# Kernel optimization log

Measured on AMD Instinct MI355X. Metric: run time of the kernel, lower is better.

Reference implementation:

```python
import jax, jax.numpy as jnp
import numpy as np
from jax import lax

D_MODEL = 256
N_LAYERS = 4
D_STATE = 64
EXPAND = 2
HEADDIM = 64
D_CONV = 4
D_INNER = EXPAND * D_MODEL                      # 512
NHEADS = D_INNER // HEADDIM                     # 8
CONV_DIM = D_INNER + 2 * D_STATE                # 640 (ngroups=1)
D_IN_PROJ = 2 * D_INNER + 2 * D_STATE + NHEADS  # 1160
B_SZ, SEQ = 8, 2048


def _silu(x):
    return x * jax.nn.sigmoid(x)


def _mamba2(u, W_in, W_conv, b_conv, dt_bias, A_log, Dp, norm_w, W_out):
    # Standard Mamba2 block (in_proj -> causal depthwise conv -> selective scan
    # with per-head scalar A -> gated RMSNorm -> out_proj).
    B, L, _ = u.shape
    zxbcdt = u @ W_in.T                                   # [B,L,1160]
    z = zxbcdt[..., :D_INNER]
    xBC = zxbcdt[..., D_INNER:D_INNER + CONV_DIM]
    dt = jax.nn.softplus(zxbcdt[..., D_INNER + CONV_DIM:] + dt_bias)  # [B,L,H]
    # causal depthwise conv1d + silu
    xc = lax.conv_general_dilated(xBC.transpose(0, 2, 1), W_conv[:, None, :],
                                  (1,), [(D_CONV - 1, 0)],
                                  dimension_numbers=('NCH', 'OIH', 'NCH'),
                                  feature_group_count=CONV_DIM)
    xBC = _silu(xc.transpose(0, 2, 1) + b_conv)
    x = xBC[..., :D_INNER].reshape(B, L, NHEADS, HEADDIM)
    Bm = xBC[..., D_INNER:D_INNER + D_STATE]              # [B,L,N]
    Cm = xBC[..., D_INNER + D_STATE:]                     # [B,L,N]
    dA = jnp.exp(dt * (-jnp.exp(A_log)))                  # [B,L,H]

    def step(h, inp):
        dA_t, dt_t, x_t, B_t, C_t = inp
        # h: [B,H,P,N]
        h = dA_t[:, :, None, None] * h + (dt_t[:, :, None] * x_t)[..., None] * B_t[:, None, None, :]
        y = jnp.einsum('bhpn,bn->bhp', h, C_t)
        return h, y

    h0 = jnp.zeros((B, NHEADS, HEADDIM, D_STATE), u.dtype)
    xs = (dA.transpose(1, 0, 2), dt.transpose(1, 0, 2), x.transpose(1, 0, 2, 3),
          Bm.transpose(1, 0, 2), Cm.transpose(1, 0, 2))
    _, ys = lax.scan(step, h0, xs)                        # [L,B,H,P]
    y = ys.transpose(1, 0, 2, 3) + Dp[None, None, :, None] * x
    y = y.reshape(B, L, D_INNER)
    y = y * _silu(z)                                      # gate before RMSNorm
    y = y * lax.rsqrt(jnp.mean(y * y, axis=-1, keepdims=True) + 1e-5) * norm_w
    return y @ W_out.T


def _encoder(x, pf, pb):
    for i in range(N_LAYERS - 1):
        y_fwd = _mamba2(x, *[p[i] for p in pf])
        y_bwd = _mamba2(x[:, ::-1], *[p[i] for p in pb])[:, ::-1]
        x = y_fwd + y_bwd
    h_fwd = _mamba2(x, *[p[-1] for p in pf])
    h_bwd = _mamba2(x[:, ::-1], *[p[-1] for p in pb])[:, ::-1]
    H = (h_fwd + h_bwd).mean(axis=1)
    return h_fwd, h_bwd, H


def _make_params(key):
    k = jax.random.split(key, 4)
    W_in = jax.random.normal(k[0], (N_LAYERS, D_IN_PROJ, D_MODEL), jnp.float32) * 0.02
    W_conv = jax.random.normal(k[1], (N_LAYERS, CONV_DIM, D_CONV), jnp.float32) * 0.2
    b_conv = jnp.zeros((N_LAYERS, CONV_DIM), jnp.float32)
    dt = jnp.exp(jax.random.uniform(k[2], (N_LAYERS, NHEADS)) * (np.log(0.1) - np.log(0.001)) + np.log(0.001))
    dt_bias = dt + jnp.log(-jnp.expm1(-dt))               # softplus^{-1}(dt)
    A_log = jnp.log(jax.random.uniform(k[3], (N_LAYERS, NHEADS), minval=1.0, maxval=16.0))
    Dp = jnp.ones((N_LAYERS, NHEADS), jnp.float32)
    norm_w = jnp.ones((N_LAYERS, D_INNER), jnp.float32)
    W_out = jax.random.normal(jax.random.fold_in(k[0], 7), (N_LAYERS, D_MODEL, D_INNER), jnp.float32) * 0.02
    return (W_in, W_conv, b_conv, dt_bias, A_log, Dp, norm_w, W_out)


def setup_inputs():
    key = jax.random.key(0)
    kx, kf, kb = jax.random.split(key, 3)
    x = jax.random.normal(kx, (B_SZ, SEQ, D_MODEL), jnp.float32)
    pf = _make_params(kf)
    pb = _make_params(kb)
    names = ['Win', 'Wconv', 'bconv', 'dt_bias', 'A_log', 'D', 'norm_w', 'Wout']
    inp = {'x_conditioned': x}
    for n, p in zip(names, pf):
        inp[n + '_f'] = p
    for n, p in zip(names, pb):
        inp[n + '_b'] = p
    return inp


def reference(x_conditioned, Win_f, Wconv_f, bconv_f, dt_bias_f, A_log_f, D_f, norm_w_f, Wout_f,
              Win_b, Wconv_b, bconv_b, dt_bias_b, A_log_b, D_b, norm_w_b, Wout_b):
    pf = (Win_f, Wconv_f, bconv_f, dt_bias_f, A_log_f, D_f, norm_w_f, Wout_f)
    pb = (Win_b, Wconv_b, bconv_b, dt_bias_b, A_log_b, D_b, norm_w_b, Wout_b)
    return _encoder(x_conditioned, pf, pb)
```

## Files before the change

### kernel.cpp

```cpp
#include <hip/hip_runtime.h>
#include <math.h>


#define TC 64
#define NC 32
#define SPITCH 72
#define HIOFF 8388608

#define ZB_STR   8388608u
#define XBCB_STR 10485760u
#define HINP_STR 16777216u
#define XCP_STR  10485760u
#define DT_STR   131072u
#define SB_STR   131072u
#define PT_STR   2048u

typedef __attribute__((ext_vector_type(4))) float f32x4;
typedef __attribute__((ext_vector_type(8))) short s16x8;

#define MFMA __builtin_amdgcn_mfma_f32_16x16x32_bf16

__device__ __forceinline__ float siluf(float x) { return x / (1.f + expf(-x)); }

__device__ __forceinline__ ushort f2b(float f) {
  union { float f; uint u; } v; v.f = f;
  return (ushort)((v.u + 0x7FFFu + ((v.u >> 16) & 1u)) >> 16);
}
__device__ __forceinline__ float b2f(ushort u) {
  union { uint u; float f; } v; v.u = ((uint)u) << 16; return v.f;
}
__device__ __forceinline__ int swz(int r, int c) { return c ^ (r & 3) ^ ((r >> 2) & 3); }

__device__ __forceinline__ int soff(int base, int r, int cc) {
  return base + r * SPITCH + ((((cc >> 3) ^ (r & 7) ^ ((r >> 3) & 7)) << 3) | (cc & 7));
}
__device__ __forceinline__ int toff(int base, int r, int cc) {
  return base + r * 64 + ((((cc >> 3) ^ (r & 7)) << 3) | (cc & 7));
}

__device__ __forceinline__ uint packf(float y) {
  const ushort hb = f2b(y);
  const ushort lb = f2b(y - b2f(hb));
  return (uint)hb | ((uint)lb << 16);
}
__device__ __forceinline__ float unpackf(uint u) {
  return b2f((ushort)(u & 0xffffu)) + b2f((ushort)(u >> 16));
}

__device__ __forceinline__ void unzip8(const uint4 u0, const uint4 u1, s16x8& hh, s16x8& ll) {
  const uint a[8] = {u0.x, u0.y, u0.z, u0.w, u1.x, u1.y, u1.z, u1.w};
#pragma unroll
  for (int e = 0; e < 8; ++e) {
    hh[e] = (short)(a[e] & 0xffffu);
    ll[e] = (short)(a[e] >> 16);
  }
}

__device__ __forceinline__ void stage16p(ushort* tiles, const uint* src,
                                         int bh_, int bl_, int r, int c0) {
  const uint4 u0 = *(const uint4*)(src + c0);
  const uint4 u1 = *(const uint4*)(src + c0 + 4);
  const uint4 u2 = *(const uint4*)(src + c0 + 8);
  const uint4 u3 = *(const uint4*)(src + c0 + 12);
  s16x8 h0, l0, h1, l1;
  unzip8(u0, u1, h0, l0);
  unzip8(u2, u3, h1, l1);
  *(s16x8*)&tiles[toff(bh_, r, c0)]     = h0;
  *(s16x8*)&tiles[toff(bl_, r, c0)]     = l0;
  *(s16x8*)&tiles[toff(bh_, r, c0 + 8)] = h1;
  *(s16x8*)&tiles[toff(bl_, r, c0 + 8)] = l1;
}

__global__ __launch_bounds__(256) void k_cvt(
    const float* __restrict__ src, ushort* __restrict__ dst, int n8)
{
  const int i = blockIdx.x * 256 + threadIdx.x;
  if (i >= n8) return;
  const float4 v0 = *(const float4*)(src + (size_t)i * 8);
  const float4 v1 = *(const float4*)(src + (size_t)i * 8 + 4);
  s16x8 h;
#pragma unroll
  for (int e = 0; e < 4; ++e) h[e] = (short)f2b(((const float*)&v0)[e]);
#pragma unroll
  for (int e = 0; e < 4; ++e) h[e + 4] = (short)f2b(((const float*)&v1)[e]);
  *(s16x8*)(dst + (size_t)i * 8) = h;
}

__global__ __launch_bounds__(256) void k_gemmb(
    const ushort* __restrict__ A, const ushort* __restrict__ Winb, int layer,
    ushort* __restrict__ zb, ushort* __restrict__ xbc,
    const float* __restrict__ db0, const float* __restrict__ db1,
    const float* __restrict__ Al0, const float* __restrict__ Al1,
    float* __restrict__ dtb, float* __restrict__ dab)
{
  const int zd = blockIdx.z;
  const ushort* W = Winb + ((size_t)zd * 4 + layer) * 296960;
  zb  += (size_t)zd * ZB_STR;
  xbc += (size_t)zd * XBCB_STR;
  dtb += (size_t)zd * DT_STR;
  dab += (size_t)zd * DT_STR;
  const float* dt_bias = zd ? db1 : db0;
  const float* A_log   = zd ? Al1 : Al0;
  const int N = 1160, K = 256;

  __shared__ __align__(16) ushort lds[17408];
  const int tid = threadIdx.x;
  const int lane = tid & 63;
  const int wid = tid >> 6;
  const int wr = wid >> 1, wc = wid & 1;
  const int m0 = blockIdx.x * 128, n0 = blockIdx.y * 128;

  const int tr = tid >> 1;
  const int th = tid & 1;
  const int gm = m0 + tr;
  const int bb = gm >> 11, tt = gm & 2047;
  const int tphys = zd ? (2047 - tt) : tt;
  const ushort* Arow = A + (size_t)((bb << 11) + tphys) * 256 + th * 16;
  const int wn = n0 + tr;
  const ushort* Wrow = (wn < N) ? (W + (size_t)wn * K + th * 16) : nullptr;

  const int asw0 = tr * 32 + swz(tr, th * 2) * 8;
  const int asw1 = tr * 32 + swz(tr, th * 2 + 1) * 8;

  f32x4 acc[4][4];
#pragma unroll
  for (int i = 0; i < 4; ++i)
#pragma unroll
    for (int j = 0; j < 4; ++j) acc[i][j] = (f32x4){0.f, 0.f, 0.f, 0.f};

  int aoff[4], boff[4];
#pragma unroll
  for (int f = 0; f < 4; ++f) {
    const int ar = wr * 64 + f * 16 + (lane & 15);
    aoff[f] = ar * 32 + swz(ar, lane >> 4) * 8;
    const int br = wc * 64 + f * 16 + (lane & 15);
    boff[f] = 4096 + br * 32 + swz(br, lane >> 4) * 8;
  }

  const s16x8 zz = (s16x8){0, 0, 0, 0, 0, 0, 0, 0};
  s16x8 a0 = *(const s16x8*)(Arow);
  s16x8 a1 = *(const s16x8*)(Arow + 8);
  s16x8 b0 = zz, b1 = zz;
  if (Wrow) {
    b0 = *(const s16x8*)(Wrow);
    b1 = *(const s16x8*)(Wrow + 8);
  }

  for (int k0 = 0; k0 < K; k0 += 32) {
    __syncthreads();
    *(s16x8*)&lds[asw0] = a0;
    *(s16x8*)&lds[asw1] = a1;
    *(s16x8*)&lds[4096 + asw0] = b0;
    *(s16x8*)&lds[4096 + asw1] = b1;
    __syncthreads();
    if (k0 + 32 < K) {
      a0 = *(const s16x8*)(Arow + k0 + 32);
      a1 = *(const s16x8*)(Arow + k0 + 40);
      if (Wrow) {
        b0 = *(const s16x8*)(Wrow + k0 + 32);
        b1 = *(const s16x8*)(Wrow + k0 + 40);
      }
    }
    s16x8 af[4], bf[4];
#pragma unroll
    for (int f = 0; f < 4; ++f) {
      af[f] = *(const s16x8*)&lds[aoff[f]];
      bf[f] = *(const s16x8*)&lds[boff[f]];
    }
#pragma unroll
    for (int i = 0; i < 4; ++i)
#pragma unroll
      for (int j = 0; j < 4; ++j)
        acc[i][j] = MFMA(af[i], bf[j], acc[i][j], 0, 0, 0);
  }

  const int by = blockIdx.y;
  if (by == 9) {
    if (wc == 0 && (lane & 15) < 8) {
      const int cl = lane & 15;
      const float bias = dt_bias[cl];
      const float eAl = expf(A_log[cl]);
#pragma unroll
      for (int i = 0; i < 4; ++i) {
        const int r = m0 + wr * 64 + i * 16 + (lane >> 4) * 4;
#pragma unroll
        for (int g = 0; g < 4; ++g) {
          const float v = acc[i][0][g] + bias;
          const float sp = (v > 20.f) ? v : log1pf(expf(v));
          dtb[(size_t)(r + g) * 8 + cl] = sp;
          dab[(size_t)(r + g) * 8 + cl] = sp * eAl;
        }
      }
    }
    return;
  }
  __syncthreads();
#pragma unroll
  for (int i = 0; i < 4; ++i) {
    const int r = wr * 64 + i * 16 + (lane >> 4) * 4;
#pragma unroll
    for (int j = 0; j < 4; ++j) {
      const int ccol = wc * 64 + j * 16 + (lane & 15);
#pragma unroll
      for (int g = 0; g < 4; ++g)
        lds[(r + g) * 136 + ccol] = f2b(acc[i][j][g]);
    }
  }
  __syncthreads();
  const int rr = tid >> 1, hf = tid & 1;
  const int grow = m0 + rr;
  ushort* dst; int stride, colb;
  if (by < 4) { dst = zb;  stride = 512; colb = n0; }
  else        { dst = xbc; stride = 640; colb = n0 - 512; }
  ushort* dp = dst + (size_t)grow * stride + colb + hf * 64;
  const ushort* sp = &lds[rr * 136 + hf * 64];
#pragma unroll
  for (int q = 0; q < 8; ++q)
    *(s16x8*)(dp + q * 8) = *(const s16x8*)(sp + q * 8);
}

__global__ __launch_bounds__(256) void k_gemmo_mid(
    const ushort* __restrict__ ybf, const ushort* __restrict__ Woutb, int layer,
    ushort* __restrict__ xbf)
{
  __shared__ __align__(16) ushort lds[8192];
  const int tid = threadIdx.x;
  const int lane = tid & 63;
  const int wid = tid >> 6;
  const int wr = wid >> 1, wc = wid & 1;
  const int m0 = blockIdx.x * 128, n0 = blockIdx.y * 128;

  const int tr = tid >> 1;
  const int th = tid & 1;
  const int gm = m0 + tr;
  const int bb = gm >> 11, tt = gm & 2047;
  const int wn = n0 + tr;

  const int asw0 = tr * 32 + swz(tr, th * 2) * 8;
  const int asw1 = tr * 32 + swz(tr, th * 2 + 1) * 8;

  f32x4 acc[4][4];
#pragma unroll
  for (int i = 0; i < 4; ++i)
#pragma unroll
    for (int j = 0; j < 4; ++j) acc[i][j] = (f32x4){0.f, 0.f, 0.f, 0.f};

  int aoff[4], boff[4];
#pragma unroll
  for (int f = 0; f < 4; ++f) {
    const int ar = wr * 64 + f * 16 + (lane & 15);
    aoff[f] = ar * 32 + swz(ar, lane >> 4) * 8;
    const int br = wc * 64 + f * 16 + (lane & 15);
    boff[f] = 4096 + br * 32 + swz(br, lane >> 4) * 8;
  }

  for (int dir = 0; dir < 2; ++dir) {
    const int tphys = dir ? (2047 - tt) : tt;
    const ushort* Arow = ybf + (size_t)dir * ZB_STR
                       + (size_t)((bb << 11) + tphys) * 512 + th * 16;
    const ushort* Wrow = Woutb + ((size_t)dir * 4 + layer) * 131072
                       + (size_t)wn * 512 + th * 16;
    s16x8 a0 = *(const s16x8*)(Arow);
    s16x8 a1 = *(const s16x8*)(Arow + 8);
    s16x8 b0 = *(const s16x8*)(Wrow);
    s16x8 b1 = *(const s16x8*)(Wrow + 8);
    for (int k0 = 0; k0 < 512; k0 += 32) {
      __syncthreads();
      *(s16x8*)&lds[asw0] = a0;
      *(s16x8*)&lds[asw1] = a1;
      *(s16x8*)&lds[4096 + asw0] = b0;
      *(s16x8*)&lds[4096 + asw1] = b1;
      __syncthreads();
      if (k0 + 32 < 512) {
        a0 = *(const s16x8*)(Arow + k0 + 32);
        a1 = *(const s16x8*)(Arow + k0 + 40);
        b0 = *(const s16x8*)(Wrow + k0 + 32);
        b1 = *(const s16x8*)(Wrow + k0 + 40);
      }
      s16x8 af[4], bf[4];
#pragma unroll
      for (int f = 0; f < 4; ++f) {
        af[f] = *(const s16x8*)&lds[aoff[f]];
        bf[f] = *(const s16x8*)&lds[boff[f]];
      }
#pragma unroll
      for (int i = 0; i < 4; ++i)
#pragma unroll
        for (int j = 0; j < 4; ++j)
          acc[i][j] = MFMA(af[i], bf[j], acc[i][j], 0, 0, 0);
    }
  }

#pragma unroll
  for (int i = 0; i < 4; ++i) {
    const int rb = m0 + wr * 64 + i * 16 + (lane >> 4) * 4;
#pragma unroll
    for (int g = 0; g < 4; ++g) {
      const size_t rbase = (size_t)(rb + g) * 256 + n0 + wc * 64 + (lane & 15);
#pragma unroll
      for (int j = 0; j < 4; ++j)
        xbf[rbase + j * 16] = f2b(acc[i][j][g]);
    }
  }
}

__global__ __launch_bounds__(256) void k_gemmo_last(
    const ushort* __restrict__ ybf, const ushort* __restrict__ Woutb,
    float* __restrict__ hF, float* __restrict__ hB)
{
  const int zd = blockIdx.z;
  const ushort* A = ybf + (size_t)zd * ZB_STR;
  const ushort* W = Woutb + ((size_t)zd * 4 + 3) * 131072;
  float* Cout = zd ? hB : hF;

  __shared__ __align__(16) ushort lds[8192];
  const int tid = threadIdx.x;
  const int lane = tid & 63;
  const int wid = tid >> 6;
  const int wr = wid >> 1, wc = wid & 1;
  const int m0 = blockIdx.x * 128, n0 = blockIdx.y * 128;

  const int tr = tid >> 1;
  const int th = tid & 1;
  const int gm = m0 + tr;
  const ushort* Arow = A + (size_t)gm * 512 + th * 16;
  const int wn = n0 + tr;
  const ushort* Wrow = W + (size_t)wn * 512 + th * 16;

  const int asw0 = tr * 32 + swz(tr, th * 2) * 8;
  const int asw1 = tr * 32 + swz(tr, th * 2 + 1) * 8;

  f32x4 acc[4][4];
#pragma unroll
  for (int i = 0; i < 4; ++i)
#pragma unroll
    for (int j = 0; j < 4; ++j) acc[i][j] = (f32x4){0.f, 0.f, 0.f, 0.f};

  int aoff[4], boff[4];
#pragma unroll
  for (int f = 0; f < 4; ++f) {
    const int ar = wr * 64 + f * 16 + (lane & 15);
    aoff[f] = ar * 32 + swz(ar, lane >> 4) * 8;
    const int br = wc * 64 + f * 16 + (lane & 15);
    boff[f] = 4096 + br * 32 + swz(br, lane >> 4) * 8;
  }

  s16x8 a0 = *(const s16x8*)(Arow);
  s16x8 a1 = *(const s16x8*)(Arow + 8);
  s16x8 b0 = *(const s16x8*)(Wrow);
  s16x8 b1 = *(const s16x8*)(Wrow + 8);

  for (int k0 = 0; k0 < 512; k0 += 32) {
    __syncthreads();
    *(s16x8*)&lds[asw0] = a0;
    *(s16x8*)&lds[asw1] = a1;
    *(s16x8*)&lds[4096 + asw0] = b0;
    *(s16x8*)&lds[4096 + asw1] = b1;
    __syncthreads();
    if (k0 + 32 < 512) {
      a0 = *(const s16x8*)(Arow + k0 + 32);
      a1 = *(const s16x8*)(Arow + k0 + 40);
      b0 = *(const s16x8*)(Wrow + k0 + 32);
      b1 = *(const s16x8*)(Wrow + k0 + 40);
    }
    s16x8 af[4], bf[4];
#pragma unroll
    for (int f = 0; f < 4; ++f) {
      af[f] = *(const s16x8*)&lds[aoff[f]];
      bf[f] = *(const s16x8*)&lds[boff[f]];
    }
#pragma unroll
    for (int i = 0; i < 4; ++i)
#pragma unroll
      for (int j = 0; j < 4; ++j)
        acc[i][j] = MFMA(af[i], bf[j], acc[i][j], 0, 0, 0);
  }

#pragma unroll
  for (int i = 0; i < 4; ++i) {
    const int rb = m0 + wr * 64 + i * 16 + (lane >> 4) * 4;
#pragma unroll
    for (int g = 0; g < 4; ++g) {
      const int row = rb + g;
      const int b2_ = row >> 11, t2 = row & 2047;
      const int tw = zd ? (2047 - t2) : t2;
      float* crow = Cout + ((size_t)((b2_ << 11) + tw)) * 256 + n0 + wc * 64 + (lane & 15);
#pragma unroll
      for (int j = 0; j < 4; ++j)
        crow[j * 16] = acc[i][j][g];
    }
  }
}

__global__ __launch_bounds__(256) void k_conv(
    const ushort* __restrict__ xbc,
    const float* __restrict__ Wc0, const float* __restrict__ Wc1,
    const float* __restrict__ bc0, const float* __restrict__ bc1,
    uint* __restrict__ xcp)
{
  const int zd = blockIdx.z;
  xbc += (size_t)zd * XBCB_STR;
  xcp += (size_t)zd * XCP_STR;
  const float* Wc = zd ? Wc1 : Wc0;
  const float* bc = zd ? bc1 : bc0;

  const int t = threadIdx.x;
  const int cg = blockIdx.x * 8 + (t & 7);
  const int c0 = cg * 8;
  const int rt0 = (blockIdx.y * 32 + (t >> 3)) * 16;

  float4 wv[8];
  const float4* wp = (const float4*)(Wc + c0 * 4);
#pragma unroll
  for (int e = 0; e < 8; ++e) wv[e] = wp[e];
  float bias[8];
#pragma unroll
  for (int e = 0; e < 8; ++e) bias[e] = bc[c0 + e];

  const s16x8 zz = (s16x8){0, 0, 0, 0, 0, 0, 0, 0};
  s16x8 w0, w1, w2;
  {
    const int l0 = rt0 & 2047;
    w0 = (l0 >= 3) ? *(const s16x8*)(xbc + (size_t)(rt0 - 3) * 640 + c0) : zz;
    w1 = (l0 >= 2) ? *(const s16x8*)(xbc + (size_t)(rt0 - 2) * 640 + c0) : zz;
    w2 = (l0 >= 1) ? *(const s16x8*)(xbc + (size_t)(rt0 - 1) * 640 + c0) : zz;
  }

#pragma unroll 4
  for (int i = 0; i < 16; ++i) {
    const int row = rt0 + i;
    const s16x8 cur = *(const s16x8*)(xbc + (size_t)row * 640 + c0);
    uint o[8];
#pragma unroll
    for (int e = 0; e < 8; ++e) {
      const float* w = (const float*)&wv[e];
      float a = bias[e];
      a = fmaf(b2f((ushort)w0[e]), w[0], a);
      a = fmaf(b2f((ushort)w1[e]), w[1], a);
      a = fmaf(b2f((ushort)w2[e]), w[2], a);
      a = fmaf(b2f((ushort)cur[e]), w[3], a);
      o[e] = packf(siluf(a));
    }
    uint* op = xcp + (size_t)row * 640 + c0;
    *(uint4*)op = make_uint4(o[0], o[1], o[2], o[3]);
    *(uint4*)(op + 4) = make_uint4(o[4], o[5], o[6], o[7]);
    w0 = w1; w1 = w2; w2 = cur;
  }
}

__global__ __launch_bounds__(256) void k_scan1(
    uint* __restrict__ xcp, const float* __restrict__ dt,
    const float* __restrict__ dtA,
    const float* __restrict__ Dp0, const float* __restrict__ Dp1,
    ushort* __restrict__ hin, float* __restrict__ Sbuf,
    float* __restrict__ PT)
{
  const int zd = blockIdx.z;
  xcp  += (size_t)zd * XCP_STR;
  dt   += (size_t)zd * DT_STR;
  dtA  += (size_t)zd * DT_STR;
  hin  += (size_t)zd * HINP_STR;
  Sbuf += (size_t)zd * SB_STR;
  PT   += (size_t)zd * PT_STR;
  const float* Dp = zd ? Dp1 : Dp0;

  const int c = blockIdx.x & (NC - 1);
  const int bhi = blockIdx.x >> 5;
  const int b = bhi >> 3, h = bhi & 7;
  const int tid = threadIdx.x;
  const int lane = tid & 63;
  const int wid = tid >> 6;
  const int r0 = b * 2048 + c * TC;
  const int hbase = h * 64;
  __shared__ __align__(16) ushort tiles[24576];
  __shared__ float Ssh[64], dtsh[64], vsh[64];
  enum { PCH = 0, PCL = 4096, PBH = 8192, PBL = 12288, PXH = 16384, PXL = 20480 };

  if (tid < 64) {
    float a = dtA[(size_t)(r0 + tid) * 8 + h];
    const float d = dt[(size_t)(r0 + tid) * 8 + h];
#pragma unroll
    for (int off = 1; off < 64; off <<= 1) {
      const float t = __shfl_up(a, off);
      if (tid >= off) a += t;
    }
    const float slast = __shfl(a, 63);
    Ssh[tid] = a;
    dtsh[tid] = d;
    vsh[tid] = expf(a - slast) * d;
    Sbuf[(size_t)bhi * 2048 + c * TC + tid] = a;
    if (tid == 63) PT[bhi * NC + c] = expf(-slast);
  }
  {
    const int r = tid >> 2, c0 = (tid & 3) * 16;
    const uint* rowp = xcp + (size_t)(r0 + r) * 640;
    stage16p(tiles, rowp + 512, PBH, PBL, r, c0);
    stage16p(tiles, rowp + 576, PCH, PCL, r, c0);
    stage16p(tiles, rowp + hbase, PXH, PXL, r, c0);
  }
  __syncthreads();

  const int ib = wid * 16;
  const int frow = lane & 15;
  const int fkc = lane >> 4;

  const int tp = tid >> 2;
  const int tj0 = (tid & 3) * 16;
  s16x8 xtr[4], btr[4];
#pragma unroll
  for (int cc = 0; cc < 2; ++cc) {
    const int j0 = tj0 + cc * 8;
    s16x8 vh, vl, wh, wl;
#pragma unroll
    for (int e = 0; e < 8; ++e) {
      const int ax = toff(PXH, j0 + e, tp);
      vh[e] = (short)tiles[ax];
      vl[e] = (short)tiles[ax + 4096];
      const int ab = toff(PBH, j0 + e, tp);
      wh[e] = (short)tiles[ab];
      wl[e] = (short)tiles[ab + 4096];
    }
    xtr[cc] = vh; xtr[cc + 2] = vl;
    btr[cc] = wh; btr[cc + 2] = wl;
  }

  s16x8 pah[2], pal[2];
#pragma unroll
  for (int ks = 0; ks < 2; ++ks) {
    pah[ks] = *(const s16x8*)&tiles[toff(PCH, ib + frow, ks * 32 + fkc * 8)];
    pal[ks] = *(const s16x8*)&tiles[toff(PCL, ib + frow, ks * 32 + fkc * 8)];
  }
  f32x4 acc[4];
#pragma unroll
  for (int jt = 0; jt < 4; ++jt) acc[jt] = (f32x4){0.f, 0.f, 0.f, 0.f};
#pragma unroll
  for (int jt = 0; jt < 4; ++jt) {
#pragma unroll
    for (int ks = 0; ks < 2; ++ks) {
      const s16x8 tbh = *(const s16x8*)&tiles[toff(PBH, jt * 16 + frow, ks * 32 + fkc * 8)];
      const s16x8 tbl = *(const s16x8*)&tiles[toff(PBL, jt * 16 + frow, ks * 32 + fkc * 8)];
      acc[jt] = MFMA(pah[ks], tbh, acc[jt], 0, 0, 0);
      acc[jt] = MFMA(pah[ks], tbl, acc[jt], 0, 0, 0);
      acc[jt] = MFMA(pal[ks], tbh, acc[jt], 0, 0, 0);
    }
  }
  float Si[4];
#pragma unroll
  for (int g = 0; g < 4; ++g) Si[g] = Ssh[ib + fkc * 4 + g];
#pragma unroll
  for (int jt = 0; jt < 4; ++jt) {
    const int j = jt * 16 + frow;
    const float Sj = Ssh[j], dj = dtsh[j];
#pragma unroll
    for (int g = 0; g < 4; ++g) {
      const int i = ib + fkc * 4 + g;
      const float w = (j <= i) ? __expf(Sj - Si[g]) * dj : 0.f;
      const float gt = acc[jt][g] * w;
      const ushort gh = f2b(gt);
      tiles[toff(PCH, i, j)] = gh;
      tiles[toff(PCL, i, j)] = f2b(gt - b2f(gh));
    }
  }
  __syncthreads();

#pragma unroll
  for (int cc = 0; cc < 2; ++cc) {
    *(s16x8*)&tiles[toff(PXH, tp, tj0 + cc * 8)] = xtr[cc];
    *(s16x8*)&tiles[toff(PXL, tp, tj0 + cc * 8)] = xtr[cc + 2];
    *(s16x8*)&tiles[toff(PBH, tp, tj0 + cc * 8)] = btr[cc];
    *(s16x8*)&tiles[toff(PBL, tp, tj0 + cc * 8)] = btr[cc + 2];
  }
  __syncthreads();

  s16x8 gah[2], gal[2];
#pragma unroll
  for (int ks = 0; ks < 2; ++ks) {
    gah[ks] = *(const s16x8*)&tiles[toff(PCH, ib + frow, ks * 32 + fkc * 8)];
    gal[ks] = *(const s16x8*)&tiles[toff(PCL, ib + frow, ks * 32 + fkc * 8)];
  }
  const float dpv = Dp[h];
#pragma unroll
  for (int pt = 0; pt < 4; ++pt) {
    f32x4 accY = (f32x4){0.f, 0.f, 0.f, 0.f};
#pragma unroll
    for (int ks = 0; ks < 2; ++ks) {
      const s16x8 xh = *(const s16x8*)&tiles[toff(PXH, pt * 16 + frow, ks * 32 + fkc * 8)];
      const s16x8 xl = *(const s16x8*)&tiles[toff(PXL, pt * 16 + frow, ks * 32 + fkc * 8)];
      accY = MFMA(gah[ks], xh, accY, 0, 0, 0);
      accY = MFMA(gah[ks], xl, accY, 0, 0, 0);
      accY = MFMA(gal[ks], xh, accY, 0, 0, 0);
    }
    const int p = pt * 16 + frow;
#pragma unroll
    for (int g = 0; g < 4; ++g) {
      const int i = ib + fkc * 4 + g;
      const int ax = toff(PXH, p, i);
      const float xv = b2f(tiles[ax]) + b2f(tiles[ax + 4096]);
      xcp[(size_t)(r0 + i) * 640 + hbase + p] = packf(accY[g] + dpv * xv);
    }
  }

  s16x8 xvh[2], xvl[2];
#pragma unroll
  for (int ks = 0; ks < 2; ++ks) {
    const int J0 = ks * 32 + fkc * 8;
    const s16x8 xh = *(const s16x8*)&tiles[toff(PXH, ib + frow, J0)];
    const s16x8 xl = *(const s16x8*)&tiles[toff(PXL, ib + frow, J0)];
#pragma unroll
    for (int e = 0; e < 8; ++e) {
      const float xf = (b2f((ushort)xh[e]) + b2f((ushort)xl[e])) * vsh[J0 + e];
      const ushort nh = f2b(xf);
      xvh[ks][e] = (short)nh;
      xvl[ks][e] = (short)f2b(xf - b2f(nh));
    }
  }
  ushort* hbp = hin + (((size_t)(bhi * NC + c)) << 12);
#pragma unroll
  for (int nt = 0; nt < 4; ++nt) {
    f32x4 accC = (f32x4){0.f, 0.f, 0.f, 0.f};
#pragma unroll
    for (int ks = 0; ks < 2; ++ks) {
      const s16x8 tbh = *(const s16x8*)&tiles[toff(PBH, nt * 16 + frow, ks * 32 + fkc * 8)];
      const s16x8 tbl = *(const s16x8*)&tiles[toff(PBL, nt * 16 + frow, ks * 32 + fkc * 8)];
      accC = MFMA(xvh[ks], tbh, accC, 0, 0, 0);
      accC = MFMA(xvh[ks], tbl, accC, 0, 0, 0);
      accC = MFMA(xvl[ks], tbh, accC, 0, 0, 0);
    }
    const int n = nt * 16 + frow;
    const int kss = nt >> 1;
    const int nlo3 = (n >> 3) & 3, ne = n & 7;
#pragma unroll
    for (int g = 0; g < 4; ++g) {
      const int plo = fkc * 4 + g;
      const int off = ((wid * 2 + kss) << 9) + (nlo3 * 16 + plo) * 8 + ne;
      const float v = accC[g];
      const ushort vh = f2b(v);
      hbp[off] = vh;
      hbp[off + HIOFF] = f2b(v - b2f(vh));
    }
  }
}

__global__ __launch_bounds__(256) void k_scan2(
    ushort* __restrict__ hin, const float* __restrict__ PT)
{
  const int zd = blockIdx.z;
  hin += (size_t)zd * HINP_STR;
  PT  += (size_t)zd * PT_STR;
  const int bh = blockIdx.x >> 2, jt = blockIdx.x & 3;
  const int t = threadIdx.x;
  float hv[4] = {0.f, 0.f, 0.f, 0.f};
  for (int c = 0; c < NC; ++c) {
    ushort* base = hin + (((size_t)(bh * NC + c)) << 12) + (jt << 10) + t * 4;
    const float pt = PT[bh * NC + c];
    const ushort4 uh = *(const ushort4*)base;
    const ushort4 ul = *(const ushort4*)(base + HIOFF);
    const float vals[4] = {b2f(uh.x) + b2f(ul.x), b2f(uh.y) + b2f(ul.y),
                           b2f(uh.z) + b2f(ul.z), b2f(uh.w) + b2f(ul.w)};
    ushort4 nh, nl;
    ushort* nhp = (ushort*)&nh; ushort* nlp = (ushort*)&nl;
#pragma unroll
    for (int k = 0; k < 4; ++k) {
      const float old = hv[k];
      hv[k] = fmaf(pt, hv[k], vals[k]);
      const ushort oh = f2b(old);
      nhp[k] = oh;
      nlp[k] = f2b(old - b2f(oh));
    }
    *(ushort4*)base = nh;
    *(ushort4*)(base + HIOFF) = nl;
  }
}

__global__ __launch_bounds__(512) void k_scan3f(
    const uint* __restrict__ xcp, const ushort* __restrict__ z,
    const ushort* __restrict__ hin, const float* __restrict__ Sbuf,
    const float* __restrict__ nw0, const float* __restrict__ nw1,
    ushort* __restrict__ ybf)
{
  const int zd = blockIdx.z;
  xcp  += (size_t)zd * XCP_STR;
  z    += (size_t)zd * ZB_STR;
  hin  += (size_t)zd * HINP_STR;
  Sbuf += (size_t)zd * SB_STR;
  ybf  += (size_t)zd * ZB_STR;
  const float* normw = zd ? nw1 : nw0;

  const int c = blockIdx.x & (NC - 1);
  const int b = blockIdx.x >> 5;
  const int tid = threadIdx.x;
  const int lane = tid & 63;
  const int h = tid >> 6;
  const int r0 = b * 2048 + c * TC;
  const int frow = lane & 15;
  const int fk = (lane >> 4) * 8;
  __shared__ __align__(16) ushort ybuf[64 * 524];
  __shared__ float Esh[8][64];
  __shared__ float partial[64][9];
  __shared__ float scale[64];

  {
    const int r = tid >> 3, c0 = (tid & 7) * 8;
    const uint* rowp = xcp + (size_t)(r0 + r) * 640 + 576 + c0;
    const uint4 u0 = *(const uint4*)rowp;
    const uint4 u1 = *(const uint4*)(rowp + 4);
    s16x8 hh, ll;
    unzip8(u0, u1, hh, ll);
    *(s16x8*)&ybuf[soff(0, r, c0)]    = hh;
    *(s16x8*)&ybuf[soff(4608, r, c0)] = ll;
  }
  Esh[h][lane] = expf(-Sbuf[(size_t)((b * 8 + h) << 11) + c * TC + lane]);
  __syncthreads();

  const size_t cbase = ((size_t)((b * 8 + h) * NC + c)) << 12;
  s16x8 Bh[4][2], Bl[4][2];
  const ushort* hb = hin + cbase + lane * 8;
#pragma unroll
  for (int jt = 0; jt < 4; ++jt)
#pragma unroll
    for (int ks = 0; ks < 2; ++ks) {
      Bh[jt][ks] = *(const s16x8*)(hb + ((jt * 2 + ks) << 9));
      Bl[jt][ks] = *(const s16x8*)(hb + ((jt * 2 + ks) << 9) + HIOFF);
    }
  s16x8 Ah[4][2], Al[4][2];
#pragma unroll
  for (int it = 0; it < 4; ++it)
#pragma unroll
    for (int ks = 0; ks < 2; ++ks) {
      Ah[it][ks] = *(const s16x8*)&ybuf[soff(0, it * 16 + frow, ks * 32 + fk)];
      Al[it][ks] = *(const s16x8*)&ybuf[soff(4608, it * 16 + frow, ks * 32 + fk)];
    }

  f32x4 acc[4][4];
#pragma unroll
  for (int it = 0; it < 4; ++it)
#pragma unroll
    for (int jt = 0; jt < 4; ++jt) acc[it][jt] = (f32x4){0.f, 0.f, 0.f, 0.f};
#pragma unroll
  for (int it = 0; it < 4; ++it)
#pragma unroll
    for (int jt = 0; jt < 4; ++jt)
#pragma unroll
      for (int ks = 0; ks < 2; ++ks) {
        acc[it][jt] = MFMA(Ah[it][ks], Bh[jt][ks], acc[it][jt], 0, 0, 0);
        acc[it][jt] = MFMA(Ah[it][ks], Bl[jt][ks], acc[it][jt], 0, 0, 0);
        acc[it][jt] = MFMA(Al[it][ks], Bh[jt][ks], acc[it][jt], 0, 0, 0);
      }

  float rowsq[4][4];
#pragma unroll
  for (int it = 0; it < 4; ++it)
#pragma unroll
    for (int g = 0; g < 4; ++g) rowsq[it][g] = 0.f;
#pragma unroll
  for (int it = 0; it < 4; ++it)
#pragma unroll
    for (int jt = 0; jt < 4; ++jt) {
      const int gcol = h * 64 + jt * 16 + frow;
#pragma unroll
      for (int g = 0; g < 4; ++g) {
        const int row = it * 16 + (lane >> 4) * 4 + g;
        const float yl = unpackf(xcp[(size_t)(r0 + row) * 640 + gcol]);
        const float zf = b2f(z[(size_t)(r0 + row) * 512 + gcol]);
        const float y = (yl + Esh[h][row] * acc[it][jt][g]) * siluf(zf);
        acc[it][jt][g] = y;
        rowsq[it][g] = fmaf(y, y, rowsq[it][g]);
      }
    }
#pragma unroll
  for (int it = 0; it < 4; ++it)
#pragma unroll
    for (int g = 0; g < 4; ++g) {
      float s = rowsq[it][g];
      s += __shfl_xor(s, 1);
      s += __shfl_xor(s, 2);
      s += __shfl_xor(s, 4);
      s += __shfl_xor(s, 8);
      if (frow == 0) partial[it * 16 + (lane >> 4) * 4 + g][h] = s;
    }
  __syncthreads();
  if (tid < 64) {
    float s = 0.f;
#pragma unroll
    for (int hh = 0; hh < 8; ++hh) s += partial[tid][hh];
    scale[tid] = rsqrtf(s * (1.f / 512.f) + 1e-5f);
  }
  __syncthreads();

  float wreg[4];
#pragma unroll
  for (int jt = 0; jt < 4; ++jt) wreg[jt] = normw[h * 64 + jt * 16 + frow];
#pragma unroll
  for (int it = 0; it < 4; ++it)
#pragma unroll
    for (int jt = 0; jt < 4; ++jt) {
      const int col = h * 64 + jt * 16 + frow;
#pragma unroll
      for (int g = 0; g < 4; ++g) {
        const int row = it * 16 + (lane >> 4) * 4 + g;
        ybuf[row * 524 + col] = f2b(acc[it][jt][g] * scale[row] * wreg[jt]);
      }
    }
  __syncthreads();
#pragma unroll
  for (int j = 0; j < 8; ++j) {
    const int flat = j * 4096 + tid * 8;
    const int row = flat >> 9, col = flat & 511;
    const ushort4 u0 = *(const ushort4*)&ybuf[row * 524 + col];
    const ushort4 u1 = *(const ushort4*)&ybuf[row * 524 + col + 4];
    s16x8 o;
    o[0] = (short)u0.x; o[1] = (short)u0.y; o[2] = (short)u0.z; o[3] = (short)u0.w;
    o[4] = (short)u1.x; o[5] = (short)u1.y; o[6] = (short)u1.z; o[7] = (short)u1.w;
    *(s16x8*)(ybf + (size_t)(r0 + row) * 512 + col) = o;
  }
}

__global__ __launch_bounds__(256) void k_hpart(
    const float* __restrict__ hf, const float* __restrict__ hb,
    float* __restrict__ part)
{
  const int g = blockIdx.x;
  const int b = g >> 5, seg = g & 31;
  const int m = threadIdx.x;
  float s = 0.f;
  for (int l = seg * 64; l < seg * 64 + 64; ++l) {
    const size_t idx = ((size_t)b * 2048 + l) * 256 + m;
    s += hf[idx] + hb[idx];
  }
  part[(size_t)g * 256 + m] = s;
}

__global__ __launch_bounds__(256) void k_hfinal(
    const float* __restrict__ part, float* __restrict__ H)
{
  const int b = blockIdx.x;
  const int m = threadIdx.x;
  float s = 0.f;
  for (int g = 0; g < 32; ++g) s += part[(size_t)(b * 32 + g) * 256 + m];
  H[b * 256 + m] = s * (1.f / 2048.f);
}

extern "C" void kernel_launch(void* const* d_in, const int* in_sizes, int n_in,
                              void* d_out, int out_size, void* d_ws, size_t ws_size,
                              hipStream_t stream) {
  const float* x_in = (const float*)d_in[0];
  const float* Win[2]    = {(const float*)d_in[1],  (const float*)d_in[9]};
  const float* Wconv[2]  = {(const float*)d_in[2],  (const float*)d_in[10]};
  const float* bconv[2]  = {(const float*)d_in[3],  (const float*)d_in[11]};
  const float* dtbias[2] = {(const float*)d_in[4],  (const float*)d_in[12]};
  const float* Alog[2]   = {(const float*)d_in[5],  (const float*)d_in[13]};
  const float* Dpar[2]   = {(const float*)d_in[6],  (const float*)d_in[14]};
  const float* normw[2]  = {(const float*)d_in[7],  (const float*)d_in[15]};
  const float* Wout[2]   = {(const float*)d_in[8],  (const float*)d_in[16]};

  float* ws = (float*)d_ws;
  ushort* zb    = (ushort*)ws;
  ushort* ybf   = zb;
  ushort* xbcb  = (ushort*)(ws + 8388608);
  ushort* hinp  = (ushort*)(ws + 18874368);
  uint* xcp     = (uint*)(ws + 35651584);
  float* dtb     = ws + 56623104;
  float* dab     = ws + 56885248;
  float* Sbuf    = ws + 57147392;
  float* PT      = ws + 57409536;
  float* part    = ws + 57413632;
  ushort* xbf    = (ushort*)(ws + 57479168);
  ushort* Winb   = (ushort*)(ws + 59576320);
  ushort* Woutb  = (ushort*)(ws + 60764160);

  float* hF = (float*)d_out;
  float* hB = hF + (size_t)8 * 2048 * 256;
  float* Hm = hB + (size_t)8 * 2048 * 256;

  k_cvt<<<580, 256, 0, stream>>>(Win[0], Winb, 148480);
  k_cvt<<<580, 256, 0, stream>>>(Win[1], Winb + 1187840, 148480);
  k_cvt<<<256, 256, 0, stream>>>(Wout[0], Woutb, 65536);
  k_cvt<<<256, 256, 0, stream>>>(Wout[1], Woutb + 524288, 65536);
  k_cvt<<<2048, 256, 0, stream>>>(x_in, xbf, 524288);

  for (int layer = 0; layer < 4; ++layer) {
    const float* Wc0 = Wconv[0] + (size_t)layer * 640 * 4;
    const float* Wc1 = Wconv[1] + (size_t)layer * 640 * 4;
    const float* bc0 = bconv[0] + (size_t)layer * 640;
    const float* bc1 = bconv[1] + (size_t)layer * 640;

    k_gemmb<<<dim3(128, 10, 2), 256, 0, stream>>>(
        xbf, Winb, layer, zb, xbcb,
        dtbias[0] + layer * 8, dtbias[1] + layer * 8,
        Alog[0] + layer * 8, Alog[1] + layer * 8, dtb, dab);
    k_conv<<<dim3(10, 32, 2), 256, 0, stream>>>(xbcb, Wc0, Wc1, bc0, bc1, xcp);
    k_scan1<<<dim3(2048, 1, 2), 256, 0, stream>>>(
        xcp, dtb, dab, Dpar[0] + layer * 8, Dpar[1] + layer * 8,
        hinp, Sbuf, PT);
    k_scan2<<<dim3(256, 1, 2), 256, 0, stream>>>(hinp, PT);
    k_scan3f<<<dim3(256, 1, 2), 512, 0, stream>>>(
        xcp, zb, hinp, Sbuf,
        normw[0] + layer * 512, normw[1] + layer * 512, ybf);
    if (layer < 3) {
      k_gemmo_mid<<<dim3(128, 2), 256, 0, stream>>>(ybf, Woutb, layer, xbf);
    } else {
      k_gemmo_last<<<dim3(128, 2, 2), 256, 0, stream>>>(ybf, Woutb, hF, hB);
    }
  }
  k_hpart<<<256, 256, 0, stream>>>(hF, hB, part);
  k_hfinal<<<8, 256, 0, stream>>>(part, Hm);
}
```

Baseline: 1.006 ms.

## Pack hi/lo state halves into one word and halve gemmo_mid row tile

The inter-chunk state buffer used to store its bf16 hi and lo halves as two separate arrays placed far apart. They now sit together as one packed 32-bit word per element, so scan1, scan2 and scan3f each issue one contiguous access per element instead of two distant ones. Separately, k_gemmo_mid now uses 64-row M tiles instead of 128, doubling the grid to 512 blocks so more CUs are busy. The cost is more reads of the weight tile across blocks and an extra unzip step in scan3f.

```diff
diff --git a/kernel.cpp b/kernel.cpp
--- a/kernel.cpp
+++ b/kernel.cpp
@@ -5,11 +5,10 @@
 #define TC 64
 #define NC 32
 #define SPITCH 72
-#define HIOFF 8388608
 
 #define ZB_STR   8388608u
 #define XBCB_STR 10485760u
-#define HINP_STR 16777216u
+#define HINPU_STR 8388608u
 #define XCP_STR  10485760u
 #define DT_STR   131072u
 #define SB_STR   131072u
@@ -223,68 +222,68 @@
     const ushort* __restrict__ ybf, const ushort* __restrict__ Woutb, int layer,
     ushort* __restrict__ xbf)
 {
-  __shared__ __align__(16) ushort lds[8192];
+  __shared__ __align__(16) ushort lds[6144];
   const int tid = threadIdx.x;
   const int lane = tid & 63;
   const int wid = tid >> 6;
   const int wr = wid >> 1, wc = wid & 1;
-  const int m0 = blockIdx.x * 128, n0 = blockIdx.y * 128;
-
-  const int tr = tid >> 1;
-  const int th = tid & 1;
-  const int gm = m0 + tr;
+  const int m0 = blockIdx.x * 64, n0 = blockIdx.y * 128;
+
+  const int trA = tid >> 2, kcA = tid & 3;
+  const int aswA = trA * 32 + swz(trA, kcA) * 8;
+  const int trB = tid >> 1, thB = tid & 1;
+  const int bsw0 = 2048 + trB * 32 + swz(trB, thB * 2) * 8;
+  const int bsw1 = 2048 + trB * 32 + swz(trB, thB * 2 + 1) * 8;
+
+  const int gm = m0 + trA;
   const int bb = gm >> 11, tt = gm & 2047;
-  const int wn = n0 + tr;
-
-  const int asw0 = tr * 32 + swz(tr, th * 2) * 8;
-  const int asw1 = tr * 32 + swz(tr, th * 2 + 1) * 8;
-
-  f32x4 acc[4][4];
-#pragma unroll
-  for (int i = 0; i < 4; ++i)
+  const int wn = n0 + trB;
+
+  f32x4 acc[2][4];
+#pragma unroll
+  for (int i = 0; i < 2; ++i)
 #pragma unroll
     for (int j = 0; j < 4; ++j) acc[i][j] = (f32x4){0.f, 0.f, 0.f, 0.f};
 
-  int aoff[4], boff[4];
-#pragma unroll
-  for (int f = 0; f < 4; ++f) {
-    const int ar = wr * 64 + f * 16 + (lane & 15);
+  int aoff[2], boff[4];
+#pragma unroll
+  for (int f = 0; f < 2; ++f) {
+    const int ar = wr * 32 + f * 16 + (lane & 15);
     aoff[f] = ar * 32 + swz(ar, lane >> 4) * 8;
-    const int br = wc * 64 + f * 16 + (lane & 15);
-    boff[f] = 4096 + br * 32 + swz(br, lane >> 4) * 8;
+  }
+#pragma unroll
+  for (int j = 0; j < 4; ++j) {
+    const int br = wc * 64 + j * 16 + (lane & 15);
+    boff[j] = 2048 + br * 32 + swz(br, lane >> 4) * 8;
   }
 
   for (int dir = 0; dir < 2; ++dir) {
     const int tphys = dir ? (2047 - tt) : tt;
     const ushort* Arow = ybf + (size_t)dir * ZB_STR
-                       + (size_t)((bb << 11) + tphys) * 512 + th * 16;
+                       + (size_t)((bb << 11) + tphys) * 512 + kcA * 8;
     const ushort* Wrow = Woutb + ((size_t)dir * 4 + layer) * 131072
-                       + (size_t)wn * 512 + th * 16;
+                       + (size_t)wn * 512 + thB * 16;
     s16x8 a0 = *(const s16x8*)(Arow);
-    s16x8 a1 = *(const s16x8*)(Arow + 8);
     s16x8 b0 = *(const s16x8*)(Wrow);
     s16x8 b1 = *(const s16x8*)(Wrow + 8);
     for (int k0 = 0; k0 < 512; k0 += 32) {
       __syncthreads();
-      *(s16x8*)&lds[asw0] = a0;
-      *(s16x8*)&lds[asw1] = a1;
-      *(s16x8*)&lds[4096 + asw0] = b0;
-      *(s16x8*)&lds[4096 + asw1] = b1;
+      *(s16x8*)&lds[aswA] = a0;
+      *(s16x8*)&lds[bsw0] = b0;
+      *(s16x8*)&lds[bsw1] = b1;
       __syncthreads();
       if (k0 + 32 < 512) {
         a0 = *(const s16x8*)(Arow + k0 + 32);
-        a1 = *(const s16x8*)(Arow + k0 + 40);
         b0 = *(const s16x8*)(Wrow + k0 + 32);
         b1 = *(const s16x8*)(Wrow + k0 + 40);
       }
-      s16x8 af[4], bf[4];
-#pragma unroll
-      for (int f = 0; f < 4; ++f) {
-        af[f] = *(const s16x8*)&lds[aoff[f]];
-        bf[f] = *(const s16x8*)&lds[boff[f]];
-      }
-#pragma unroll
-      for (int i = 0; i < 4; ++i)
+      s16x8 af[2], bf[4];
+#pragma unroll
+      for (int f = 0; f < 2; ++f) af[f] = *(const s16x8*)&lds[aoff[f]];
+#pragma unroll
+      for (int j = 0; j < 4; ++j) bf[j] = *(const s16x8*)&lds[boff[j]];
+#pragma unroll
+      for (int i = 0; i < 2; ++i)
 #pragma unroll
         for (int j = 0; j < 4; ++j)
           acc[i][j] = MFMA(af[i], bf[j], acc[i][j], 0, 0, 0);
@@ -292,8 +291,8 @@
   }
 
 #pragma unroll
-  for (int i = 0; i < 4; ++i) {
-    const int rb = m0 + wr * 64 + i * 16 + (lane >> 4) * 4;
+  for (int i = 0; i < 2; ++i) {
+    const int rb = m0 + wr * 32 + i * 16 + (lane >> 4) * 4;
 #pragma unroll
     for (int g = 0; g < 4; ++g) {
       const size_t rbase = (size_t)(rb + g) * 256 + n0 + wc * 64 + (lane & 15);
@@ -452,14 +451,14 @@
     uint* __restrict__ xcp, const float* __restrict__ dt,
     const float* __restrict__ dtA,
     const float* __restrict__ Dp0, const float* __restrict__ Dp1,
-    ushort* __restrict__ hin, float* __restrict__ Sbuf,
+    uint* __restrict__ hin, float* __restrict__ Sbuf,
     float* __restrict__ PT)
 {
   const int zd = blockIdx.z;
   xcp  += (size_t)zd * XCP_STR;
   dt   += (size_t)zd * DT_STR;
   dtA  += (size_t)zd * DT_STR;
-  hin  += (size_t)zd * HINP_STR;
+  hin  += (size_t)zd * HINPU_STR;
   Sbuf += (size_t)zd * SB_STR;
   PT   += (size_t)zd * PT_STR;
   const float* Dp = zd ? Dp1 : Dp0;
@@ -614,7 +613,7 @@
       xvl[ks][e] = (short)f2b(xf - b2f(nh));
     }
   }
-  ushort* hbp = hin + (((size_t)(bhi * NC + c)) << 12);
+  uint* hbp = hin + (((size_t)(bhi * NC + c)) << 12);
 #pragma unroll
   for (int nt = 0; nt < 4; ++nt) {
     f32x4 accC = (f32x4){0.f, 0.f, 0.f, 0.f};
@@ -633,55 +632,47 @@
     for (int g = 0; g < 4; ++g) {
       const int plo = fkc * 4 + g;
       const int off = ((wid * 2 + kss) << 9) + (nlo3 * 16 + plo) * 8 + ne;
-      const float v = accC[g];
-      const ushort vh = f2b(v);
-      hbp[off] = vh;
-      hbp[off + HIOFF] = f2b(v - b2f(vh));
+      hbp[off] = packf(accC[g]);
     }
   }
 }
 
 __global__ __launch_bounds__(256) void k_scan2(
-    ushort* __restrict__ hin, const float* __restrict__ PT)
+    uint* __restrict__ hin, const float* __restrict__ PT)
 {
   const int zd = blockIdx.z;
-  hin += (size_t)zd * HINP_STR;
+  hin += (size_t)zd * HINPU_STR;
   PT  += (size_t)zd * PT_STR;
   const int bh = blockIdx.x >> 2, jt = blockIdx.x & 3;
   const int t = threadIdx.x;
   float hv[4] = {0.f, 0.f, 0.f, 0.f};
   for (int c = 0; c < NC; ++c) {
-    ushort* base = hin + (((size_t)(bh * NC + c)) << 12) + (jt << 10) + t * 4;
+    uint* base = hin + (((size_t)(bh * NC + c)) << 12) + (jt << 10) + t * 4;
     const float pt = PT[bh * NC + c];
-    const ushort4 uh = *(const ushort4*)base;
-    const ushort4 ul = *(const ushort4*)(base + HIOFF);
-    const float vals[4] = {b2f(uh.x) + b2f(ul.x), b2f(uh.y) + b2f(ul.y),
-                           b2f(uh.z) + b2f(ul.z), b2f(uh.w) + b2f(ul.w)};
-    ushort4 nh, nl;
-    ushort* nhp = (ushort*)&nh; ushort* nlp = (ushort*)&nl;
+    const uint4 u = *(const uint4*)base;
+    const float vals[4] = {unpackf(u.x), unpackf(u.y), unpackf(u.z), unpackf(u.w)};
+    uint4 nv;
+    uint* nvp = (uint*)&nv;
 #pragma unroll
     for (int k = 0; k < 4; ++k) {
       const float old = hv[k];
       hv[k] = fmaf(pt, hv[k], vals[k]);
-      const ushort oh = f2b(old);
-      nhp[k] = oh;
-      nlp[k] = f2b(old - b2f(oh));
-    }
-    *(ushort4*)base = nh;
-    *(ushort4*)(base + HIOFF) = nl;
+      nvp[k] = packf(old);
+    }
+    *(uint4*)base = nv;
   }
 }
 
 __global__ __launch_bounds__(512) void k_scan3f(
     const uint* __restrict__ xcp, const ushort* __restrict__ z,
-    const ushort* __restrict__ hin, const float* __restrict__ Sbuf,
+    const uint* __restrict__ hin, const float* __restrict__ Sbuf,
     const float* __restrict__ nw0, const float* __restrict__ nw1,
     ushort* __restrict__ ybf)
 {
   const int zd = blockIdx.z;
   xcp  += (size_t)zd * XCP_STR;
   z    += (size_t)zd * ZB_STR;
-  hin  += (size_t)zd * HINP_STR;
+  hin  += (size_t)zd * HINPU_STR;
   Sbuf += (size_t)zd * SB_STR;
   ybf  += (size_t)zd * ZB_STR;
   const float* normw = zd ? nw1 : nw0;
@@ -714,13 +705,15 @@
 
   const size_t cbase = ((size_t)((b * 8 + h) * NC + c)) << 12;
   s16x8 Bh[4][2], Bl[4][2];
-  const ushort* hb = hin + cbase + lane * 8;
+  const uint* hb = hin + cbase + lane * 8;
 #pragma unroll
   for (int jt = 0; jt < 4; ++jt)
 #pragma unroll
     for (int ks = 0; ks < 2; ++ks) {
-      Bh[jt][ks] = *(const s16x8*)(hb + ((jt * 2 + ks) << 9));
-      Bl[jt][ks] = *(const s16x8*)(hb + ((jt * 2 + ks) << 9) + HIOFF);
+      const uint* p = hb + ((jt * 2 + ks) << 9);
+      const uint4 u0 = *(const uint4*)p;
+      const uint4 u1 = *(const uint4*)(p + 4);
+      unzip8(u0, u1, Bh[jt][ks], Bl[jt][ks]);
     }
   s16x8 Ah[4][2], Al[4][2];
 #pragma unroll
@@ -857,7 +850,7 @@
   ushort* zb    = (ushort*)ws;
   ushort* ybf   = zb;
   ushort* xbcb  = (ushort*)(ws + 8388608);
-  ushort* hinp  = (ushort*)(ws + 18874368);
+  uint* hinp    = (uint*)(ws + 18874368);
   uint* xcp     = (uint*)(ws + 35651584);
   float* dtb     = ws + 56623104;
   float* dab     = ws + 56885248;
@@ -897,7 +890,7 @@
         xcp, zb, hinp, Sbuf,
         normw[0] + layer * 512, normw[1] + layer * 512, ybf);
     if (layer < 3) {
-      k_gemmo_mid<<<dim3(128, 2), 256, 0, stream>>>(ybf, Woutb, layer, xbf);
+      k_gemmo_mid<<<dim3(256, 2), 256, 0, stream>>>(ybf, Woutb, layer, xbf);
     } else {
       k_gemmo_last<<<dim3(128, 2, 2), 256, 0, stream>>>(ybf, Woutb, hF, hB);
     }
```

New measurement: 1.041 ms. 1.03x slower.
